# Optimization experiments

Hardware: AMD Instinct MI355X
Metric: run time of the kernel (lower is better)

The kernel has to match this reference:

```python
import jax, jax.numpy as jnp
import numpy as np

A, B, N, FEAT, H, R, E_PER, NACT = 3, 4096, 64, 32, 32, 6, 1536, 16


def setup_inputs() -> dict:
    key = jax.random.key(0)
    ks = jax.random.split(key, 12)
    s = 0.1
    return {
        "unary": jax.random.normal(ks[0], (A, B, N, FEAT), jnp.float32),
        "actions": jax.random.normal(ks[1], (A, B, NACT), jnp.float32),
        "w_rel": jax.random.normal(ks[2], (R, FEAT, H), jnp.float32) * s,
        "w_root": jax.random.normal(ks[3], (FEAT, H), jnp.float32) * s,
        "b_gnn": jax.random.normal(ks[4], (H,), jnp.float32) * s,
        "w1": jax.random.normal(ks[5], (A, H + NACT * (A - 1), H), jnp.float32) * s,
        "b1": jax.random.normal(ks[6], (A, H), jnp.float32) * s,
        "w2": jax.random.normal(ks[7], (A, H, NACT), jnp.float32) * s,
        "b2": jax.random.normal(ks[8], (A, NACT), jnp.float32) * s,
        "edge_src": jax.random.randint(ks[9], (E_PER,), 0, N, jnp.int32),
        "edge_dst": jax.random.randint(ks[10], (E_PER,), 0, N, jnp.int32),
        "edge_rel": jax.random.randint(ks[11], (E_PER,), 0, R, jnp.int32),
    }


def reference(unary, actions, w_rel, w_root, b_gnn, w1, b1, w2, b2,
              edge_src, edge_dst, edge_rel):
    NT = B * N  # total nodes in the batched graph
    # Replicate the shared per-graph edge list across the batch with node offsets
    offs = (jnp.arange(B, dtype=jnp.int32) * N)[:, None]
    src = (edge_src[None, :] + offs).reshape(-1)            # [E]
    dst = (edge_dst[None, :] + offs).reshape(-1)            # [E]
    rel = jnp.tile(edge_rel, B)                             # [E]
    seg = dst * R + rel                                     # per (node, relation) segment
    cnt = jax.ops.segment_sum(jnp.ones_like(rel, jnp.float32), seg,
                              num_segments=NT * R)
    inv_deg = 1.0 / jnp.maximum(cnt, 1.0)                   # RGCN mean per relation
    norm_e = inv_deg[seg][:, None]

    def rgcn_relu(x):  # x: [NT, FEAT]
        h_stack = jnp.einsum('ni,rio->rno', x, w_rel)       # [R, NT, H]
        msg = h_stack[rel, src] * norm_e                    # [E, H] gather-transform
        agg = jax.ops.segment_sum(msg, dst, num_segments=NT)
        return jax.nn.relu(agg + x @ w_root + b_gnn)

    qs = []
    for a in range(A):
        h = rgcn_relu(unary[a].reshape(NT, FEAT))           # [NT, H]
        pooled = h.reshape(B, N, H).max(axis=1)             # global max pool per graph
        others = jnp.concatenate([actions[j] for j in range(A) if j != a], axis=1)
        critic_in = jnp.concatenate([pooled, others], axis=1)
        mid = jax.nn.leaky_relu(critic_in @ w1[a] + b1[a], negative_slope=0.01)
        all_q = mid @ w2[a] + b2[a]                         # [B, NACT]
        idx = jnp.argmax(actions[a], axis=1)[:, None]
        qs.append(jnp.take_along_axis(all_q, idx, axis=1))  # [B, 1]
    return jnp.stack(qs)                                    # [A, B, 1]
```

## Files before the change

kernel.cpp:

```cpp
#include <hip/hip_runtime.h>
#include <hip/hip_bf16.h>
#include <math.h>

#define A_AG   3
#define Bq     4096
#define Nn     64
#define FEAT   32
#define Hh     32
#define Rr     6
#define E_PER  1536
#define NACT   16

#define KCAT   224
#define XSTRIDE 232

typedef __attribute__((ext_vector_type(8))) short          bfrag;
typedef __attribute__((ext_vector_type(4))) float          f32x4;
typedef __attribute__((ext_vector_type(8))) unsigned short u16x8;

__device__ __forceinline__ ushort f2bf(float x) {
    unsigned u = __float_as_uint(x);
    u = (u + 0x7fffu + ((u >> 16) & 1u)) >> 16;
    return (ushort)u;
}
__device__ __forceinline__ float bf2f(ushort b) {
    return __uint_as_float(((unsigned)b) << 16);
}

__global__ void prep(const float* __restrict__ w_rel,
                     const float* __restrict__ w_root,
                     const int* __restrict__ esrc,
                     const int* __restrict__ edst,
                     const int* __restrict__ erel,
                     int*    __restrict__ rs2_g,
                     float*  __restrict__ invdeg_g,
                     int*    __restrict__ entries_g,
                     ushort* __restrict__ Wt_g) {
    __shared__ int cnt[Nn * Rr];
    __shared__ int rs[Nn * Rr + 1];
    __shared__ int cur[Nn * Rr];
    const int t = threadIdx.x;

    for (int i = t; i < Nn * Rr; i += 256) cnt[i] = 0;
    __syncthreads();
    for (int e = t; e < E_PER; e += 256)
        atomicAdd(&cnt[edst[e] * Rr + erel[e]], 1);
    __syncthreads();
    if (t == 0) {
        int s = 0;
        for (int i = 0; i < Nn * Rr; ++i) { rs[i] = s; s += cnt[i]; }
        rs[Nn * Rr] = s;
    }
    __syncthreads();
    for (int i = t; i < Nn * Rr; i += 256) {
        cur[i] = rs[i];
        invdeg_g[i] = 1.0f / fmaxf((float)cnt[i], 1.0f);
    }
    for (int i = t; i < Nn * Rr + 1; i += 256) rs2_g[i] = rs[i];
    __syncthreads();
    for (int e = t; e < E_PER; e += 256) {
        const int seg = edst[e] * Rr + erel[e];
        const int pos = atomicAdd(&cur[seg], 1);
        entries_g[pos] = esrc[e];
    }
    for (int i = t; i < Hh * KCAT; i += 256) {
        const int h = i / KCAT, kk = i % KCAT;
        float v;
        if (kk < 192) v = w_rel[(((kk >> 5) * FEAT) + (kk & 31)) * Hh + h];
        else          v = w_root[(kk - 192) * Hh + h];
        Wt_g[i] = f2bf(v);
    }
}

__global__ __launch_bounds__(256) void critic_kernel(
    const float* __restrict__ unary,
    const float* __restrict__ actions,
    const float* __restrict__ b_gnn,
    const float* __restrict__ w1,
    const float* __restrict__ b1,
    const float* __restrict__ w2,
    const float* __restrict__ b2,
    const int*   __restrict__ rs2,
    const float* __restrict__ invdeg,
    const int*   __restrict__ entries,
    const ushort* __restrict__ Wt,
    float* __restrict__ out)
{
    const int b = blockIdx.x;
    const int a = blockIdx.y;
    const int t = threadIdx.x;

    __shared__ ushort xcat[Nn * XSTRIDE];
    __shared__ float pmax[4][32];
    __shared__ float cin[64];
    __shared__ float mid[32];
    __shared__ float allq[16];

    {
        const int row = t >> 2, f0 = (t & 3) * 8;
        const float* xp = unary + (((size_t)a * Bq + b) * Nn + row) * FEAT + f0;
        const float4 v0 = *(const float4*)xp;
        const float4 v1 = *(const float4*)(xp + 4);
        u16x8 pk;
        pk[0] = f2bf(v0.x); pk[1] = f2bf(v0.y); pk[2] = f2bf(v0.z); pk[3] = f2bf(v0.w);
        pk[4] = f2bf(v1.x); pk[5] = f2bf(v1.y); pk[6] = f2bf(v1.z); pk[7] = f2bf(v1.w);
        *(u16x8*)&xcat[row * XSTRIDE + 192 + f0] = pk;
    }
    __syncthreads();

    {
        const int d = t >> 2, fg = t & 3;
        const int base = d * Rr;
        int e_next = rs2[base];
        #pragma unroll
        for (int r = 0; r < Rr; ++r) {
            const int e0 = e_next;
            const int e1 = rs2[base + r + 1];
            e_next = e1;
            float s0=0.f,s1=0.f,s2=0.f,s3=0.f,s4=0.f,s5=0.f,s6=0.f,s7=0.f;
            for (int e = e0; e < e1; ++e) {
                const int src = entries[e];
                const u16x8 v = *(const u16x8*)&xcat[src * XSTRIDE + 192 + fg * 8];
                s0 += bf2f(v[0]); s1 += bf2f(v[1]); s2 += bf2f(v[2]); s3 += bf2f(v[3]);
                s4 += bf2f(v[4]); s5 += bf2f(v[5]); s6 += bf2f(v[6]); s7 += bf2f(v[7]);
            }
            const float inv = invdeg[base + r];
            u16x8 pk;
            pk[0] = f2bf(s0 * inv); pk[1] = f2bf(s1 * inv);
            pk[2] = f2bf(s2 * inv); pk[3] = f2bf(s3 * inv);
            pk[4] = f2bf(s4 * inv); pk[5] = f2bf(s5 * inv);
            pk[6] = f2bf(s6 * inv); pk[7] = f2bf(s7 * inv);
            *(u16x8*)&xcat[d * XSTRIDE + r * 32 + fg * 8] = pk;
        }
    }
    __syncthreads();

    {
        const int l  = t & 63, w = t >> 6;
        const int lr = l & 15, kg = l >> 4;
        const ushort* arow  = &xcat[(w * 16 + lr) * XSTRIDE + kg * 8];
        const ushort* bcol0 = Wt + lr * KCAT + kg * 8;
        const ushort* bcol1 = Wt + (16 + lr) * KCAT + kg * 8;
        f32x4 acc0 = {0.f, 0.f, 0.f, 0.f};
        f32x4 acc1 = {0.f, 0.f, 0.f, 0.f};
        #pragma unroll
        for (int ks = 0; ks < 7; ++ks) {
            const bfrag af = *(const bfrag*)(arow + ks * 32);
            const bfrag b0 = *(const bfrag*)(bcol0 + ks * 32);
            const bfrag b1 = *(const bfrag*)(bcol1 + ks * 32);
            acc0 = __builtin_amdgcn_mfma_f32_16x16x32_bf16(af, b0, acc0, 0, 0, 0);
            acc1 = __builtin_amdgcn_mfma_f32_16x16x32_bf16(af, b1, acc1, 0, 0, 0);
        }
        const float bg0 = b_gnn[lr], bg1 = b_gnn[16 + lr];
        float m0 = -INFINITY, m1 = -INFINITY;
        #pragma unroll
        for (int j = 0; j < 4; ++j) {
            m0 = fmaxf(m0, fmaxf(acc0[j] + bg0, 0.f));
            m1 = fmaxf(m1, fmaxf(acc1[j] + bg1, 0.f));
        }
        m0 = fmaxf(m0, __shfl_xor(m0, 16));
        m0 = fmaxf(m0, __shfl_xor(m0, 32));
        m1 = fmaxf(m1, __shfl_xor(m1, 16));
        m1 = fmaxf(m1, __shfl_xor(m1, 32));
        if (l < 16) { pmax[w][lr] = m0; pmax[w][16 + lr] = m1; }
    }
    __syncthreads();

    if (t < 32) {
        cin[t] = fmaxf(fmaxf(pmax[0][t], pmax[1][t]),
                       fmaxf(pmax[2][t], pmax[3][t]));
    } else if (t < 64) {
        const int k   = t - 32;
        const int jj  = k >> 4;
        const int col = k & 15;
        const int other = (jj == 0) ? (a == 0 ? 1 : 0) : (a == 2 ? 1 : 2);
        cin[t] = actions[((size_t)other * Bq + b) * NACT + col];
    }
    __syncthreads();

    if (t < 32) {
        float acc = b1[a * Hh + t];
        #pragma unroll
        for (int k = 0; k < 64; ++k)
            acc = fmaf(cin[k], w1[((size_t)a * 64 + k) * Hh + t], acc);
        mid[t] = acc > 0.f ? acc : 0.01f * acc;
    }
    __syncthreads();

    if (t < 16) {
        float acc = b2[a * NACT + t];
        #pragma unroll
        for (int k = 0; k < 32; ++k)
            acc = fmaf(mid[k], w2[((size_t)a * Hh + k) * NACT + t], acc);
        allq[t] = acc;
    }
    __syncthreads();

    if (t == 0) {
        const float* act = actions + ((size_t)a * Bq + b) * NACT;
        int best = 0;
        float bv = act[0];
        #pragma unroll
        for (int j = 1; j < NACT; ++j) {
            float v = act[j];
            if (v > bv) { bv = v; best = j; }
        }
        out[(size_t)a * Bq + b] = allq[best];
    }
}

extern "C" void kernel_launch(void* const* d_in, const int* in_sizes, int n_in,
                              void* d_out, int out_size, void* d_ws, size_t ws_size,
                              hipStream_t stream) {
    const float* unary   = (const float*)d_in[0];
    const float* actions = (const float*)d_in[1];
    const float* w_rel   = (const float*)d_in[2];
    const float* w_root  = (const float*)d_in[3];
    const float* b_gnn   = (const float*)d_in[4];
    const float* w1      = (const float*)d_in[5];
    const float* b1      = (const float*)d_in[6];
    const float* w2      = (const float*)d_in[7];
    const float* b2      = (const float*)d_in[8];
    const int* edge_src  = (const int*)d_in[9];
    const int* edge_dst  = (const int*)d_in[10];
    const int* edge_rel  = (const int*)d_in[11];
    float* out = (float*)d_out;

    char* ws = (char*)d_ws;
    int*    rs2_g     = (int*)(ws + 0);
    float*  invdeg_g  = (float*)(ws + 2048);
    int*    entries_g = (int*)(ws + 4096);
    ushort* Wt_g      = (ushort*)(ws + 10240);

    prep<<<1, 256, 0, stream>>>(w_rel, w_root, edge_src, edge_dst, edge_rel,
                                rs2_g, invdeg_g, entries_g, Wt_g);

    dim3 grid(Bq, A_AG);
    critic_kernel<<<grid, 256, 0, stream>>>(unary, actions, b_gnn,
                                            w1, b1, w2, b2,
                                            rs2_g, invdeg_g, entries_g, Wt_g,
                                            out);
}
```

Before: 319.7 us.

## Replace CSR edge-gather aggregation with dense normalized-adjacency MFMA matmul

The prep kernel now builds a dense bf16 normalized adjacency matrix of shape [(node,relation)+identity, src], with the mean-degree scaling folded in. Each critic block aggregates neighbour features with bf16 MFMA instructions over a transposed copy of X, instead of walking per-segment edge lists with scalar adds. This removes the irregular, data-dependent gather loop and its load imbalance. In exchange it does dense work over mostly-zero adjacency, reads the roughly 57KB adjacency from global/L2 in every block, adds a shared-memory transpose buffer, and requests 4 blocks per CU via launch bounds, which could raise register pressure or cause spills.

```diff
diff --git a/kernel.cpp b/kernel.cpp
--- a/kernel.cpp
+++ b/kernel.cpp
@@ -11,8 +11,11 @@
 #define E_PER  1536
 #define NACT   16
 
-#define KCAT   224
+#define KCAT    224
 #define XSTRIDE 232
+#define TSTRIDE 72
+#define NDR     384
+#define NEXT    448
 
 typedef __attribute__((ext_vector_type(8))) short          bfrag;
 typedef __attribute__((ext_vector_type(4))) float          f32x4;
@@ -26,44 +29,41 @@
 __device__ __forceinline__ float bf2f(ushort b) {
     return __uint_as_float(((unsigned)b) << 16);
 }
-
-__global__ void prep(const float* __restrict__ w_rel,
-                     const float* __restrict__ w_root,
-                     const int* __restrict__ esrc,
-                     const int* __restrict__ edst,
-                     const int* __restrict__ erel,
-                     int*    __restrict__ rs2_g,
-                     float*  __restrict__ invdeg_g,
-                     int*    __restrict__ entries_g,
-                     ushort* __restrict__ Wt_g) {
-    __shared__ int cnt[Nn * Rr];
-    __shared__ int rs[Nn * Rr + 1];
-    __shared__ int cur[Nn * Rr];
+__device__ __forceinline__ unsigned cvt_pk_bf16(float lo, float hi) {
+    unsigned r;
+    asm volatile("v_cvt_pk_bf16_f32 %0, %1, %2" : "=v"(r) : "v"(lo), "v"(hi));
+    return r;
+}
+
+__global__ __launch_bounds__(1024) void prep(
+        const float* __restrict__ w_rel,
+        const float* __restrict__ w_root,
+        const int* __restrict__ esrc,
+        const int* __restrict__ edst,
+        const int* __restrict__ erel,
+        float*  __restrict__ Adjf,
+        ushort* __restrict__ Adjbf,
+        ushort* __restrict__ Wt_g) {
+    __shared__ int   cnt[NDR];
+    __shared__ float invd[NEXT];
     const int t = threadIdx.x;
 
-    for (int i = t; i < Nn * Rr; i += 256) cnt[i] = 0;
-    __syncthreads();
-    for (int e = t; e < E_PER; e += 256)
+    for (int i = t; i < NDR; i += 1024) cnt[i] = 0;
+    __syncthreads();
+    for (int e = t; e < E_PER; e += 1024)
         atomicAdd(&cnt[edst[e] * Rr + erel[e]], 1);
     __syncthreads();
-    if (t == 0) {
-        int s = 0;
-        for (int i = 0; i < Nn * Rr; ++i) { rs[i] = s; s += cnt[i]; }
-        rs[Nn * Rr] = s;
-    }
-    __syncthreads();
-    for (int i = t; i < Nn * Rr; i += 256) {
-        cur[i] = rs[i];
-        invdeg_g[i] = 1.0f / fmaxf((float)cnt[i], 1.0f);
-    }
-    for (int i = t; i < Nn * Rr + 1; i += 256) rs2_g[i] = rs[i];
-    __syncthreads();
-    for (int e = t; e < E_PER; e += 256) {
-        const int seg = edst[e] * Rr + erel[e];
-        const int pos = atomicAdd(&cur[seg], 1);
-        entries_g[pos] = esrc[e];
-    }
-    for (int i = t; i < Hh * KCAT; i += 256) {
+    for (int i = t; i < NEXT; i += 1024)
+        invd[i] = (i < NDR) ? 1.0f / fmaxf((float)cnt[i], 1.0f) : 1.0f;
+    for (int i = t; i < NEXT * Nn; i += 1024) Adjf[i] = 0.f;
+    __syncthreads();
+    for (int e = t; e < E_PER; e += 1024)
+        atomicAdd(&Adjf[(edst[e] * Rr + erel[e]) * Nn + esrc[e]], 1.0f);
+    if (t < Nn) Adjf[(NDR + t) * Nn + t] = 1.0f;
+    __syncthreads();
+    for (int i = t; i < NEXT * Nn; i += 1024)
+        Adjbf[i] = f2bf(Adjf[i] * invd[i >> 6]);
+    for (int i = t; i < Hh * KCAT; i += 1024) {
         const int h = i / KCAT, kk = i % KCAT;
         float v;
         if (kk < 192) v = w_rel[(((kk >> 5) * FEAT) + (kk & 31)) * Hh + h];
@@ -72,7 +72,7 @@
     }
 }
 
-__global__ __launch_bounds__(256) void critic_kernel(
+__global__ __launch_bounds__(256, 4) void critic_kernel(
     const float* __restrict__ unary,
     const float* __restrict__ actions,
     const float* __restrict__ b_gnn,
@@ -80,9 +80,7 @@
     const float* __restrict__ b1,
     const float* __restrict__ w2,
     const float* __restrict__ b2,
-    const int*   __restrict__ rs2,
-    const float* __restrict__ invdeg,
-    const int*   __restrict__ entries,
+    const ushort* __restrict__ Adj,
     const ushort* __restrict__ Wt,
     float* __restrict__ out)
 {
@@ -90,6 +88,7 @@
     const int a = blockIdx.y;
     const int t = threadIdx.x;
 
+    __shared__ ushort Xt[FEAT * TSTRIDE];
     __shared__ ushort xcat[Nn * XSTRIDE];
     __shared__ float pmax[4][32];
     __shared__ float cin[64];
@@ -97,46 +96,69 @@
     __shared__ float allq[16];
 
     {
-        const int row = t >> 2, f0 = (t & 3) * 8;
-        const float* xp = unary + (((size_t)a * Bq + b) * Nn + row) * FEAT + f0;
-        const float4 v0 = *(const float4*)xp;
-        const float4 v1 = *(const float4*)(xp + 4);
-        u16x8 pk;
-        pk[0] = f2bf(v0.x); pk[1] = f2bf(v0.y); pk[2] = f2bf(v0.z); pk[3] = f2bf(v0.w);
-        pk[4] = f2bf(v1.x); pk[5] = f2bf(v1.y); pk[6] = f2bf(v1.z); pk[7] = f2bf(v1.w);
-        *(u16x8*)&xcat[row * XSTRIDE + 192 + f0] = pk;
+        const int f = t & 31, sg = t >> 5;
+        const float* xp = unary + ((((size_t)a * Bq + b) * Nn + sg * 8) * FEAT) + f;
+        unsigned w0 = cvt_pk_bf16(xp[0 * FEAT], xp[1 * FEAT]);
+        unsigned w1_ = cvt_pk_bf16(xp[2 * FEAT], xp[3 * FEAT]);
+        unsigned w2_ = cvt_pk_bf16(xp[4 * FEAT], xp[5 * FEAT]);
+        unsigned w3 = cvt_pk_bf16(xp[6 * FEAT], xp[7 * FEAT]);
+        uint4 v = {w0, w1_, w2_, w3};
+        *(uint4*)&Xt[f * TSTRIDE + sg * 8] = v;
     }
     __syncthreads();
 
     {
-        const int d = t >> 2, fg = t & 3;
-        const int base = d * Rr;
-        int e_next = rs2[base];
-        #pragma unroll
-        for (int r = 0; r < Rr; ++r) {
-            const int e0 = e_next;
-            const int e1 = rs2[base + r + 1];
-            e_next = e1;
-            float s0=0.f,s1=0.f,s2=0.f,s3=0.f,s4=0.f,s5=0.f,s6=0.f,s7=0.f;
-            for (int e = e0; e < e1; ++e) {
-                const int src = entries[e];
-                const u16x8 v = *(const u16x8*)&xcat[src * XSTRIDE + 192 + fg * 8];
-                s0 += bf2f(v[0]); s1 += bf2f(v[1]); s2 += bf2f(v[2]); s3 += bf2f(v[3]);
-                s4 += bf2f(v[4]); s5 += bf2f(v[5]); s6 += bf2f(v[6]); s7 += bf2f(v[7]);
+        const int l = t & 63, w = t >> 6;
+        const int lr = l & 15, kg = l >> 4;
+
+        bfrag af[2][2];
+        #pragma unroll
+        for (int mt = 0; mt < 2; ++mt)
+            #pragma unroll
+            for (int ks = 0; ks < 2; ++ks)
+                af[mt][ks] = *(const bfrag*)&Xt[(mt * 16 + lr) * TSTRIDE + ks * 32 + kg * 8];
+
+        const ushort* abase = Adj + (size_t)(w * 7 * 16 + lr) * Nn + kg * 8;
+        f32x4 acc[7][2];
+        #pragma unroll
+        for (int i = 0; i < 7; ++i) {
+            acc[i][0] = (f32x4){0.f, 0.f, 0.f, 0.f};
+            acc[i][1] = (f32x4){0.f, 0.f, 0.f, 0.f};
+        }
+        #pragma unroll
+        for (int i = 0; i < 7; ++i) {
+            const bfrag b0 = *(const bfrag*)(abase + i * 16 * Nn);
+            const bfrag b1f = *(const bfrag*)(abase + i * 16 * Nn + 32);
+            acc[i][0] = __builtin_amdgcn_mfma_f32_16x16x32_bf16(af[0][0], b0,  acc[i][0], 0, 0, 0);
+            acc[i][1] = __builtin_amdgcn_mfma_f32_16x16x32_bf16(af[1][0], b0,  acc[i][1], 0, 0, 0);
+            acc[i][0] = __builtin_amdgcn_mfma_f32_16x16x32_bf16(af[0][1], b1f, acc[i][0], 0, 0, 0);
+            acc[i][1] = __builtin_amdgcn_mfma_f32_16x16x32_bf16(af[1][1], b1f, acc[i][1], 0, 0, 0);
+        }
+        #pragma unroll
+        for (int i = 0; i < 7; ++i) {
+            const int nt = w * 7 + i;
+            const int dr = nt * 16 + lr;
+            int row, colb;
+            if (nt < 24) {
+                const int d = (dr * 10923) >> 16;
+                const int r = dr - 6 * d;
+                row = d; colb = r * 32;
+            } else {
+                row = dr - NDR; colb = 192;
             }
-            const float inv = invdeg[base + r];
-            u16x8 pk;
-            pk[0] = f2bf(s0 * inv); pk[1] = f2bf(s1 * inv);
-            pk[2] = f2bf(s2 * inv); pk[3] = f2bf(s3 * inv);
-            pk[4] = f2bf(s4 * inv); pk[5] = f2bf(s5 * inv);
-            pk[6] = f2bf(s6 * inv); pk[7] = f2bf(s7 * inv);
-            *(u16x8*)&xcat[d * XSTRIDE + r * 32 + fg * 8] = pk;
+            #pragma unroll
+            for (int mt = 0; mt < 2; ++mt) {
+                const unsigned lo = cvt_pk_bf16(acc[i][mt][0], acc[i][mt][1]);
+                const unsigned hi = cvt_pk_bf16(acc[i][mt][2], acc[i][mt][3]);
+                uint2 v = {lo, hi};
+                *(uint2*)&xcat[row * XSTRIDE + colb + mt * 16 + kg * 4] = v;
+            }
         }
     }
     __syncthreads();
 
     {
-        const int l  = t & 63, w = t >> 6;
+        const int l = t & 63, w = t >> 6;
         const int lr = l & 15, kg = l >> 4;
         const ushort* arow  = &xcat[(w * 16 + lr) * XSTRIDE + kg * 8];
         const ushort* bcol0 = Wt + lr * KCAT + kg * 8;
@@ -145,11 +167,11 @@
         f32x4 acc1 = {0.f, 0.f, 0.f, 0.f};
         #pragma unroll
         for (int ks = 0; ks < 7; ++ks) {
-            const bfrag af = *(const bfrag*)(arow + ks * 32);
-            const bfrag b0 = *(const bfrag*)(bcol0 + ks * 32);
-            const bfrag b1 = *(const bfrag*)(bcol1 + ks * 32);
-            acc0 = __builtin_amdgcn_mfma_f32_16x16x32_bf16(af, b0, acc0, 0, 0, 0);
-            acc1 = __builtin_amdgcn_mfma_f32_16x16x32_bf16(af, b1, acc1, 0, 0, 0);
+            const bfrag afr = *(const bfrag*)(arow + ks * 32);
+            const bfrag b0  = *(const bfrag*)(bcol0 + ks * 32);
+            const bfrag b1  = *(const bfrag*)(bcol1 + ks * 32);
+            acc0 = __builtin_amdgcn_mfma_f32_16x16x32_bf16(afr, b0, acc0, 0, 0, 0);
+            acc1 = __builtin_amdgcn_mfma_f32_16x16x32_bf16(afr, b1, acc1, 0, 0, 0);
         }
         const float bg0 = b_gnn[lr], bg1 = b_gnn[16 + lr];
         float m0 = -INFINITY, m1 = -INFINITY;
@@ -227,17 +249,15 @@
     float* out = (float*)d_out;
 
     char* ws = (char*)d_ws;
-    int*    rs2_g     = (int*)(ws + 0);
-    float*  invdeg_g  = (float*)(ws + 2048);
-    int*    entries_g = (int*)(ws + 4096);
-    ushort* Wt_g      = (ushort*)(ws + 10240);
-
-    prep<<<1, 256, 0, stream>>>(w_rel, w_root, edge_src, edge_dst, edge_rel,
-                                rs2_g, invdeg_g, entries_g, Wt_g);
+    ushort* Adjbf = (ushort*)(ws + 0);
+    ushort* Wt_g  = (ushort*)(ws + 57344);
+    float*  Adjf  = (float*)(ws + 71680);
+
+    prep<<<1, 1024, 0, stream>>>(w_rel, w_root, edge_src, edge_dst, edge_rel,
+                                 Adjf, Adjbf, Wt_g);
 
     dim3 grid(Bq, A_AG);
     critic_kernel<<<grid, 256, 0, stream>>>(unary, actions, b_gnn,
                                             w1, b1, w2, b2,
-                                            rs2_g, invdeg_g, entries_g, Wt_g,
-                                            out);
-}
+                                            Adjbf, Wt_g, out);
+}
```

Measured after the change: 302.4 us. 1.06x faster.
